# Optimization experiments

Hardware: AMD Instinct MI355X
Metric: run time of the kernel (lower is better)

## Reference

```python
import jax, jax.numpy as jnp
import numpy as np

EPSILON = 1.0
SIGMA = 1.0
SPRING_CONSTANT = 0.5


def setup_inputs() -> dict:
    key = jax.random.key(0)
    x = jax.random.normal(key, (4, 2048, 3), dtype=jnp.float32)
    return {"x": x}


def _pairwise_offdiag_distances(x):
    # x: (B, N, D) -> distances between all ordered pairs, diagonal removed: (B, N, N-1)
    B, N, D = x.shape
    pair_vec = x[:, :, None, :] - x[:, None, :, :]          # (B, N, N, D)
    sq = jnp.sum(pair_vec * pair_vec, axis=-1)              # (B, N, N)
    # safe sqrt (diagonal is exactly zero; it is sliced away below)
    dist = jnp.where(sq == 0, 0.0, jnp.sqrt(jnp.where(sq == 0, 1.0, sq)))
    # reshape trick from the torch source: drop the diagonal entries
    d = dist.reshape(B, N * N)[:, 1:]
    d = d.reshape(B, N - 1, N + 1)[:, :, :-1]
    return d.reshape(B, N, N - 1)                           # (B, N, N-1)


def reference(x):
    # Lennard-Jones potential (cutoff=None branch) + harmonic confinement;
    # forward() returns log_prob = -potential.
    d = _pairwise_offdiag_distances(x)                      # (B, N, N-1), all > 0
    inv = 1.0 / d
    pow6 = (SIGMA * inv) ** 6
    pair_potential = EPSILON * 4.0 * (pow6 * pow6 - pow6)
    # source multiplies by distances_inverse * distances (identity here, kept fused away)
    total_potential = jnp.sum(pair_potential, axis=(-1, -2)) / 2.0   # (B,)
    # harmonic potential about the center of mass (periodic=False)
    com = jnp.mean(x, axis=-2, keepdims=True)
    rel = x - com
    harm = 0.5 * SPRING_CONSTANT * jnp.sum(rel * rel, axis=(-1, -2))  # (B,)
    return -(total_potential + harm)
```

## Files before the change

kernel.cpp:

```cpp
#include <hip/hip_runtime.h>


#define NPART 2048
#define BATCH 4
#define TI 256
#define TJ 128
#define CI (NPART / TI)
#define CJ (NPART / TJ)
#define SPRING_K 0.5f

__global__ __launch_bounds__(256) void lj_pairs(const float* __restrict__ x,
                                                float* __restrict__ partial) {
    const int t  = threadIdx.x;
    const int ib = blockIdx.x;
    const int jb = blockIdx.y;
    const int b  = blockIdx.z;
    const float* __restrict__ xb = x + (size_t)b * NPART * 3;

    __shared__ float sx[TJ], sy[TJ], sz[TJ];
    if (t < TJ) {
        const int j = jb * TJ + t;
        sx[t] = xb[j * 3 + 0];
        sy[t] = xb[j * 3 + 1];
        sz[t] = xb[j * 3 + 2];
    }

    const int i = ib * TI + t;
    const float xi = xb[i * 3 + 0];
    const float yi = xb[i * 3 + 1];
    const float zi = xb[i * 3 + 2];
    __syncthreads();

    const int jbase = jb * TJ;
    float acc = 0.0f;
#pragma unroll 8
    for (int jj = 0; jj < TJ; ++jj) {
        const float dx = xi - sx[jj];
        const float dy = yi - sy[jj];
        const float dz = zi - sz[jj];
        const float sq = fmaf(dx, dx, fmaf(dy, dy, dz * dz));
        const float inv2 = __builtin_amdgcn_rcpf(sq);
        const float p6 = inv2 * inv2 * inv2;
        const float term = fmaf(p6, p6, -p6);
        acc += (jbase + jj == i) ? 0.0f : term;
    }
    acc *= 4.0f;

    for (int o = 32; o > 0; o >>= 1) acc += __shfl_down(acc, o, 64);
    __shared__ float wsum[4];
    const int lane = t & 63, w = t >> 6;
    if (lane == 0) wsum[w] = acc;
    __syncthreads();
    if (t == 0) {
        partial[((size_t)b * CI + ib) * CJ + jb] = wsum[0] + wsum[1] + wsum[2] + wsum[3];
    }
}

__global__ __launch_bounds__(256) void lj_finish(const float* __restrict__ x,
                                                 const float* __restrict__ partial,
                                                 float* __restrict__ out) {
    const int b = blockIdx.x;
    const int t = threadIdx.x;
    const float* __restrict__ xb = x + (size_t)b * NPART * 3;

    float sp = 0.0f;
    if (t < CI * CJ) sp = partial[(size_t)b * CI * CJ + t];

    float sxv = 0.0f, syv = 0.0f, szv = 0.0f, s2 = 0.0f;
    for (int i = t; i < NPART; i += 256) {
        const float xv = xb[3 * i + 0];
        const float yv = xb[3 * i + 1];
        const float zv = xb[3 * i + 2];
        sxv += xv; syv += yv; szv += zv;
        s2 = fmaf(xv, xv, fmaf(yv, yv, fmaf(zv, zv, s2)));
    }

    for (int o = 32; o > 0; o >>= 1) {
        sp  += __shfl_down(sp,  o, 64);
        sxv += __shfl_down(sxv, o, 64);
        syv += __shfl_down(syv, o, 64);
        szv += __shfl_down(szv, o, 64);
        s2  += __shfl_down(s2,  o, 64);
    }

    __shared__ float red[4][5];
    const int lane = t & 63, w = t >> 6;
    if (lane == 0) {
        red[w][0] = sp; red[w][1] = sxv; red[w][2] = syv; red[w][3] = szv; red[w][4] = s2;
    }
    __syncthreads();
    if (t == 0) {
        float SP = 0, SX = 0, SY = 0, SZ = 0, S2 = 0;
        for (int k = 0; k < 4; ++k) {
            SP += red[k][0]; SX += red[k][1]; SY += red[k][2]; SZ += red[k][3]; S2 += red[k][4];
        }
        const float pair = 0.5f * SP;
        const float harm = 0.5f * SPRING_K * (S2 - (SX * SX + SY * SY + SZ * SZ) * (1.0f / NPART));
        out[b] = -(pair + harm);
    }
}

extern "C" void kernel_launch(void* const* d_in, const int* in_sizes, int n_in,
                              void* d_out, int out_size, void* d_ws, size_t ws_size,
                              hipStream_t stream) {
    const float* x = (const float*)d_in[0];
    float* out = (float*)d_out;
    float* partial = (float*)d_ws;

    dim3 grid(CI, CJ, BATCH);
    lj_pairs<<<grid, 256, 0, stream>>>(x, partial);
    lj_finish<<<BATCH, 256, 0, stream>>>(x, partial, out);
}
```

Baseline: 61.82 us.

## Read j-tile directly from global and specialize diagonal guard per block

Halves the j-tile to 64 and drops the shared-memory staging and barrier: every thread reads the j coordinates straight from global memory through a uniform pointer, which the compiler can turn into scalar loads. The inner loop is fully unrolled and templated so only blocks whose j-range overlaps their i-range pay for the self-pair check. This doubles the number of blocks and partial sums and relies on scalar and cached loads to replace LDS reads.

```diff
diff --git a/kernel.cpp b/kernel.cpp
--- a/kernel.cpp
+++ b/kernel.cpp
@@ -4,10 +4,33 @@
 #define NPART 2048
 #define BATCH 4
 #define TI 256
-#define TJ 128
+#define TJ 64
 #define CI (NPART / TI)
 #define CJ (NPART / TJ)
 #define SPRING_K 0.5f
+
+template <bool GUARD>
+__device__ __forceinline__ float pair_chunk(const float* __restrict__ xj,
+                                            float xi, float yi, float zi,
+                                            int i_rel) {
+    float acc = 0.0f;
+#pragma unroll
+    for (int jj = 0; jj < TJ; ++jj) {
+        const float dx = xi - xj[3 * jj + 0];
+        const float dy = yi - xj[3 * jj + 1];
+        const float dz = zi - xj[3 * jj + 2];
+        const float sq = fmaf(dx, dx, fmaf(dy, dy, dz * dz));
+        const float inv2 = __builtin_amdgcn_rcpf(sq);
+        const float p6 = inv2 * inv2 * inv2;
+        const float term = fmaf(p6, p6, -p6);
+        if (GUARD) {
+            acc += (jj == i_rel) ? 0.0f : term;
+        } else {
+            acc += term;
+        }
+    }
+    return acc;
+}
 
 __global__ __launch_bounds__(256) void lj_pairs(const float* __restrict__ x,
                                                 float* __restrict__ partial) {
@@ -17,33 +40,17 @@
     const int b  = blockIdx.z;
     const float* __restrict__ xb = x + (size_t)b * NPART * 3;
 
-    __shared__ float sx[TJ], sy[TJ], sz[TJ];
-    if (t < TJ) {
-        const int j = jb * TJ + t;
-        sx[t] = xb[j * 3 + 0];
-        sy[t] = xb[j * 3 + 1];
-        sz[t] = xb[j * 3 + 2];
-    }
-
     const int i = ib * TI + t;
-    const float xi = xb[i * 3 + 0];
-    const float yi = xb[i * 3 + 1];
-    const float zi = xb[i * 3 + 2];
-    __syncthreads();
+    const float xi = xb[3 * i + 0];
+    const float yi = xb[3 * i + 1];
+    const float zi = xb[3 * i + 2];
 
     const int jbase = jb * TJ;
-    float acc = 0.0f;
-#pragma unroll 8
-    for (int jj = 0; jj < TJ; ++jj) {
-        const float dx = xi - sx[jj];
-        const float dy = yi - sy[jj];
-        const float dz = zi - sz[jj];
-        const float sq = fmaf(dx, dx, fmaf(dy, dy, dz * dz));
-        const float inv2 = __builtin_amdgcn_rcpf(sq);
-        const float p6 = inv2 * inv2 * inv2;
-        const float term = fmaf(p6, p6, -p6);
-        acc += (jbase + jj == i) ? 0.0f : term;
-    }
+    const float* __restrict__ xj = xb + 3 * jbase;
+    const bool overlap = (jbase >= ib * TI) && (jbase < ib * TI + TI);
+
+    float acc = overlap ? pair_chunk<true >(xj, xi, yi, zi, i - jbase)
+                        : pair_chunk<false>(xj, xi, yi, zi, 0);
     acc *= 4.0f;
 
     for (int o = 32; o > 0; o >>= 1) acc += __shfl_down(acc, o, 64);
```

Measured after the change: 62.48 us. Within noise of the previous version (+1.1%).
